# Performance work log

Measured on AMD Instinct MI355X. Metric: run time of the kernel, lower is better.

Reference implementation:

```python
import jax, jax.numpy as jnp
import numpy as np

N_BASIS = 16


def _kan_layer(x, coeffs, centers):
    # x: [b, in], coeffs: [out, in, n], centers: [n]
    mu = jnp.mean(x, axis=0)
    sd = jnp.std(x, axis=0, ddof=1)  # torch.std is unbiased by default
    xn = jnp.clip((x - mu) / (sd + 1e-6), -3.0, 3.0)
    # Gaussian RBF expansion: [b, in, n]
    basis = jnp.exp(-((xn[..., None] - centers) ** 2) / 0.5)
    return jnp.einsum('bin,oin->bo', basis, coeffs)


def setup_inputs() -> dict:
    key = jax.random.key(0)
    ks = jax.random.split(key, 6)
    B, IN, H = 16384, 256, 512
    return {
        'x': jax.random.normal(ks[0], (B, IN), jnp.float32),
        'coeffs1': jax.random.normal(ks[1], (H, IN, N_BASIS), jnp.float32) * 0.1,
        'coeffs2': jax.random.normal(ks[2], (H, H, N_BASIS), jnp.float32) * 0.1,
        'coeffs3': jax.random.normal(ks[3], (1, H, N_BASIS), jnp.float32) * 0.1,
        'skip_w': jax.random.normal(ks[4], (1, IN), jnp.float32) * 0.05,
        'skip_b': jnp.zeros((1,), jnp.float32),
    }


def reference(x, coeffs1, coeffs2, coeffs3, skip_w, skip_b):
    centers = jnp.linspace(-2.0, 2.0, N_BASIS).astype(x.dtype)
    h = jnp.tanh(_kan_layer(x, coeffs1, centers))
    h = jnp.tanh(_kan_layer(h, coeffs2, centers))
    out = _kan_layer(h, coeffs3, centers)[:, 0]  # squeeze(-1)
    skip = (x @ skip_w.T + skip_b)[:, 0]
    return out + skip
```

## Files before the change

kernel.cpp:

```cpp
#include <hip/hip_runtime.h>
#include <cstdint>
#include <cstddef>

typedef __attribute__((ext_vector_type(8))) _Float16 half8;
typedef __attribute__((ext_vector_type(4))) _Float16 half4;
typedef __attribute__((ext_vector_type(2))) __fp16   fp16x2;
typedef __attribute__((ext_vector_type(4))) float    floatx4;

static constexpr int B_ROWS = 16384;
static constexpr int IN_DIM = 256;
static constexpr int H_DIM  = 512;
static constexpr int NB     = 16;

__device__ __forceinline__ float fast_tanh(float x) {
  float ax = fabsf(x);
  float e  = __expf(2.0f * ax);
  float t  = 1.0f - 2.0f / (e + 1.0f);
  return copysignf(t, x);
}

__device__ __forceinline__ void gld16(const void* g, void* l) {
  __builtin_amdgcn_global_load_lds(
      (const __attribute__((address_space(1))) unsigned int*)g,
      (__attribute__((address_space(3))) unsigned int*)l, 16, 0, 0);
}

__global__ __launch_bounds__(256) void prep_k(const float* __restrict__ c1, _Float16* __restrict__ d1, size_t n41,
                                              const float* __restrict__ c2, _Float16* __restrict__ d2, size_t n42,
                                              const float* __restrict__ X,
                                              float* __restrict__ ps, float* __restrict__ ps2) {
  const int bx = blockIdx.x;
  if (bx < 128) {
    int c     = (bx & 3) * 64 + (threadIdx.x & 63);
    int chunk = threadIdx.x >> 6;
    int seg   = bx >> 2;
    int r0    = seg * 512;
    double s = 0.0, s2 = 0.0;
    for (int r = r0 + chunk; r < r0 + 512; r += 4) {
      float v = X[(size_t)r * IN_DIM + c];
      s += v; s2 += (double)v * (double)v;
    }
    __shared__ float Ls[256], Ls2[256];
    Ls[threadIdx.x] = (float)s; Ls2[threadIdx.x] = (float)s2;
    __syncthreads();
    if (chunk == 0) {
      int cl = threadIdx.x;
      float a  = Ls[cl]  + Ls[cl + 64]  + Ls[cl + 128]  + Ls[cl + 192];
      float b  = Ls2[cl] + Ls2[cl + 64] + Ls2[cl + 128] + Ls2[cl + 192];
      ps [(size_t)seg * IN_DIM + c] = a;
      ps2[(size_t)seg * IN_DIM + c] = b;
    }
  } else {
    size_t tot = n41 + n42;
    int nb_blocks = gridDim.x - 128;
    for (size_t i = (size_t)(bx - 128) * 256 + threadIdx.x; i < tot;
         i += (size_t)nb_blocks * 256) {
      const float4* sp; half4* dp; size_t j;
      if (i < n41) { sp = (const float4*)c1; dp = (half4*)d1; j = i; }
      else         { sp = (const float4*)c2; dp = (half4*)d2; j = i - n41; }
      float4 v = sp[j];
      int nb = (int)((j << 2) & 15);
      half4 r;
      float e0 = -2.f + (float)(nb + 0) * (4.f / 15.f);
      float e1 = -2.f + (float)(nb + 1) * (4.f / 15.f);
      float e2 = -2.f + (float)(nb + 2) * (4.f / 15.f);
      float e3 = -2.f + (float)(nb + 3) * (4.f / 15.f);
      r[0] = (_Float16)(v.x * __expf(-2.f * e0 * e0));
      r[1] = (_Float16)(v.y * __expf(-2.f * e1 * e1));
      r[2] = (_Float16)(v.z * __expf(-2.f * e2 * e2));
      r[3] = (_Float16)(v.w * __expf(-2.f * e3 * e3));
      dp[j] = r;
    }
  }
}

__global__ void stats_final_k(const float* __restrict__ ps,
                              const float* __restrict__ ps2,
                              int segs, int cols, int rows,
                              float* __restrict__ nmi, float* __restrict__ isd) {
  int c = blockIdx.x * blockDim.x + threadIdx.x;
  if (c >= cols) return;
  double s = 0.0, s2 = 0.0;
  for (int g = 0; g < segs; g++) { s += ps[(size_t)g * cols + c]; s2 += ps2[(size_t)g * cols + c]; }
  double mean = s / rows;
  double var  = (s2 - s * s / rows) / (rows - 1);
  if (var < 0.0) var = 0.0;
  float sd = (float)sqrt(var);
  float iv = 1.0f / (sd + 1e-6f);
  isd[c] = iv;
  nmi[c] = -(float)mean * iv;
}

__global__ __launch_bounds__(256, 2) void kan_gemm_fused(const float* __restrict__ X,
                                                         const float* __restrict__ nmi,
                                                         const float* __restrict__ isd,
                                                         const _Float16* __restrict__ Bm,
                                                         float* __restrict__ Hout,
                                                         float* __restrict__ psum,
                                                         float* __restrict__ psum2,
                                                         int C) {
  const int K = C << 4;
  const int steps = K >> 6;
  __shared__ __align__(16) _Float16 As[2][128 * 64];
  __shared__ __align__(16) _Float16 Bs[2][128 * 64];
  __shared__ float Rs1[2][128], Rs2[2][128];
  const int tid  = threadIdx.x;
  const int w = tid >> 6, lane = tid & 63;
  const int wm = w & 1, wn = w >> 1;
  const int lrow = lane & 15, quad = lane >> 4;
  const int row0 = blockIdx.x * 128;
  const int col0 = blockIdx.y * 128;

  const int s_row = tid >> 3;
  const int s_sl  = tid & 7;
  const int s_seg = s_sl ^ ((s_row >> 1) & 7);
  const _Float16* gB = Bm + (size_t)(col0 + s_row) * K + s_seg * 8;

  const int erow = tid >> 1, eh = tid & 1;
  const float* xp  = X   + (size_t)(row0 + erow) * C + 2 * eh;
  const float* mup = nmi + 2 * eh;
  const float* isp = isd + 2 * eh;

  floatx4 acc[4][4] = {};

  auto expand_store = [&](float2 v, float2 a, float2 b, int bufi) {
#pragma unroll
    for (int h = 0; h < 2; h++) {
      float xr = h ? v.y : v.x;
      float ii = h ? a.y : a.x;
      float bb = h ? b.y : b.x;
      float xn = fminf(fmaxf(fmaf(xr, ii, bb), -3.f), 3.f);
      float Wv = __expf(fmaf(-2.f, xn, -8.f) * xn);
      float g  = __expf((16.f / 15.f) * xn);
      float g2 = g * g, g4 = g2 * g2, g8 = g4 * g4;
      fp16x2 gg = __builtin_amdgcn_cvt_pkrtz(g2, g2);
      union { fp16x2 q[4]; half8 v8; } u0, u1;
      u0.q[0] = __builtin_amdgcn_cvt_pkrtz(Wv, Wv * g);
      u0.q[1] = u0.q[0] * gg;
      u0.q[2] = u0.q[1] * gg;
      u0.q[3] = u0.q[2] * gg;
      float W8 = Wv * g8;
      u1.q[0] = __builtin_amdgcn_cvt_pkrtz(W8, W8 * g);
      u1.q[1] = u1.q[0] * gg;
      u1.q[2] = u1.q[1] * gg;
      u1.q[3] = u1.q[2] * gg;
      int ks0 = 4 * eh + 2 * h;
      *(half8*)&As[bufi][(size_t)(ks0 * 128 + erow) * 8]       = u0.v8;
      *(half8*)&As[bufi][(size_t)((ks0 + 1) * 128 + erow) * 8] = u1.v8;
    }
  };

#pragma unroll
  for (int i = 0; i < 4; i++)
    gld16(gB + (size_t)32 * i * K, &Bs[0][(size_t)(tid + 256 * i) * 8]);
  expand_store(*(const float2*)xp, *(const float2*)isp, *(const float2*)mup, 0);
  float2 xv = {}, av = {}, bv = {};
  if (steps > 1) {
    xv = *(const float2*)(xp + 4);
    av = *(const float2*)(isp + 4);
    bv = *(const float2*)(mup + 4);
  }
  __syncthreads();

  for (int k = 0; k < steps; k++) {
    const int buf = k & 1, nb = buf ^ 1;
    const bool more = (k + 1 < steps);
    if (more) {
#pragma unroll
      for (int i = 0; i < 4; i++)
        gld16(gB + (size_t)(k + 1) * 64 + (size_t)32 * i * K,
              &Bs[nb][(size_t)(tid + 256 * i) * 8]);
    }
    half8 af0[4], bf0[4];
#pragma unroll
    for (int t = 0; t < 4; t++) {
      int arow = wm * 64 + t * 16 + lrow;
      af0[t] = *(const half8*)&As[buf][(size_t)(quad * 128 + arow) * 8];
      int brow = wn * 64 + t * 16 + lrow;
      int bchunk = brow * 8 + (quad ^ ((brow >> 1) & 7));
      bf0[t] = *(const half8*)&Bs[buf][(size_t)bchunk * 8];
    }
    __builtin_amdgcn_s_setprio(1);
#pragma unroll
    for (int tm = 0; tm < 4; tm++)
#pragma unroll
      for (int tn = 0; tn < 4; tn++)
        acc[tm][tn] = __builtin_amdgcn_mfma_f32_16x16x32_f16(af0[tm], bf0[tn], acc[tm][tn], 0, 0, 0);
    __builtin_amdgcn_s_setprio(0);
    if (more) {
      expand_store(xv, av, bv, nb);
      if (k + 2 < steps) {
        xv = *(const float2*)(xp + 4 * (k + 2));
        av = *(const float2*)(isp + 4 * (k + 2));
        bv = *(const float2*)(mup + 4 * (k + 2));
      }
    }
    half8 af1[4], bf1[4];
#pragma unroll
    for (int t = 0; t < 4; t++) {
      int arow = wm * 64 + t * 16 + lrow;
      af1[t] = *(const half8*)&As[buf][(size_t)((4 + quad) * 128 + arow) * 8];
      int brow = wn * 64 + t * 16 + lrow;
      int bchunk = brow * 8 + ((4 + quad) ^ ((brow >> 1) & 7));
      bf1[t] = *(const half8*)&Bs[buf][(size_t)bchunk * 8];
    }
    __builtin_amdgcn_s_setprio(1);
#pragma unroll
    for (int tm = 0; tm < 4; tm++)
#pragma unroll
      for (int tn = 0; tn < 4; tn++)
        acc[tm][tn] = __builtin_amdgcn_mfma_f32_16x16x32_f16(af1[tm], bf1[tn], acc[tm][tn], 0, 0, 0);
    __builtin_amdgcn_s_setprio(0);
    __syncthreads();
  }

  float s1[4] = {0.f, 0.f, 0.f, 0.f}, s2v[4] = {0.f, 0.f, 0.f, 0.f};
#pragma unroll
  for (int tm = 0; tm < 4; tm++) {
#pragma unroll
    for (int tn = 0; tn < 4; tn++) {
      int gcol = col0 + wn * 64 + tn * 16 + lrow;
#pragma unroll
      for (int r = 0; r < 4; r++) {
        int grow = row0 + wm * 64 + tm * 16 + quad * 4 + r;
        float v = fast_tanh(acc[tm][tn][r]);
        Hout[(size_t)grow * H_DIM + gcol] = v;
        s1[tn] += v; s2v[tn] += v * v;
      }
    }
  }
#pragma unroll
  for (int tn = 0; tn < 4; tn++) {
    s1[tn]  += __shfl_xor(s1[tn], 16);  s1[tn]  += __shfl_xor(s1[tn], 32);
    s2v[tn] += __shfl_xor(s2v[tn], 16); s2v[tn] += __shfl_xor(s2v[tn], 32);
  }
  if (quad == 0) {
#pragma unroll
    for (int tn = 0; tn < 4; tn++) {
      Rs1[wm][wn * 64 + tn * 16 + lrow] = s1[tn];
      Rs2[wm][wn * 64 + tn * 16 + lrow] = s2v[tn];
    }
  }
  __syncthreads();
  if (tid < 128) {
    psum [(size_t)blockIdx.x * H_DIM + col0 + tid] = Rs1[0][tid] + Rs1[1][tid];
    psum2[(size_t)blockIdx.x * H_DIM + col0 + tid] = Rs2[0][tid] + Rs2[1][tid];
  }
}

__global__ __launch_bounds__(256) void layer3_k(const float* __restrict__ H2,
                                                const float* __restrict__ nmi,
                                                const float* __restrict__ isd,
                                                const float* __restrict__ C3,
                                                const float* __restrict__ X,
                                                const float* __restrict__ SW,
                                                const float* __restrict__ SB,
                                                float* __restrict__ OUT) {
  int w = threadIdx.x >> 6, lane = threadIdx.x & 63;
  float Kn[NB];
#pragma unroll
  for (int n = 0; n < NB; n++) {
    float c = -2.f + (float)n * (4.f / 15.f);
    Kn[n] = __expf(-2.f * c * c);
  }
  float sb0 = SB[0];
  int row_base = blockIdx.x * 16 + w * 4;
  for (int r = 0; r < 4; r++) {
    int row = row_base + r;
    float s = 0.f;
#pragma unroll
    for (int j = 0; j < 8; j++) {
      int i = lane + 64 * j;
      float hv = H2[(size_t)row * H_DIM + i];
      float xn = fminf(fmaxf(fmaf(hv, isd[i], nmi[i]), -3.f), 3.f);
      float Wf = __expf(fmaf(-2.f, xn, -8.f) * xn);
      float gf = __expf((16.f / 15.f) * xn);
      const floatx4* cp = (const floatx4*)(C3 + (size_t)i * NB);
      floatx4 c0 = cp[0], c1 = cp[1], c2 = cp[2], c3 = cp[3];
      float p = Wf;
#pragma unroll
      for (int n = 0; n < 4; n++) { s += p * Kn[n]      * c0[n]; p *= gf; }
#pragma unroll
      for (int n = 0; n < 4; n++) { s += p * Kn[n + 4]  * c1[n]; p *= gf; }
#pragma unroll
      for (int n = 0; n < 4; n++) { s += p * Kn[n + 8]  * c2[n]; p *= gf; }
#pragma unroll
      for (int n = 0; n < 4; n++) { s += p * Kn[n + 12] * c3[n]; p *= gf; }
    }
#pragma unroll
    for (int j = 0; j < 4; j++) {
      int i = lane + 64 * j;
      s += X[(size_t)row * IN_DIM + i] * SW[i];
    }
#pragma unroll
    for (int off = 32; off > 0; off >>= 1) s += __shfl_down(s, off);
    if (lane == 0) OUT[row] = s + sb0;
  }
}

extern "C" void kernel_launch(void* const* d_in, const int* in_sizes, int n_in,
                              void* d_out, int out_size, void* d_ws, size_t ws_size,
                              hipStream_t stream) {
  const float* x  = (const float*)d_in[0];
  const float* c1 = (const float*)d_in[1];
  const float* c2 = (const float*)d_in[2];
  const float* c3 = (const float*)d_in[3];
  const float* sw = (const float*)d_in[4];
  const float* sb = (const float*)d_in[5];
  float* out = (float*)d_out;

  const int B = B_ROWS, IN = IN_DIM, H = H_DIM;

  char* ws = (char*)d_ws;
  size_t off = 0;
  auto alloc = [&](size_t bytes) -> void* {
    void* p = ws + off;
    off += (bytes + 255) & ~(size_t)255;
    return p;
  };
  _Float16* C1h = (_Float16*)alloc((size_t)H * IN * NB * 2);
  _Float16* C2h = (_Float16*)alloc((size_t)H * H  * NB * 2);
  float* H1 = (float*)alloc((size_t)B * H * 4);
  float* H2 = (float*)alloc((size_t)B * H * 4);
  float* ps  = (float*)alloc(128 * 512 * 4);
  float* ps2 = (float*)alloc(128 * 512 * 4);
  float* nmi = (float*)alloc(512 * 4);
  float* isd = (float*)alloc(512 * 4);

  prep_k<<<128 + 1024, 256, 0, stream>>>(c1, C1h, (size_t)H * IN * NB / 4,
                                         c2, C2h, (size_t)H * H * NB / 4,
                                         x, ps, ps2);
  stats_final_k<<<1, 256, 0, stream>>>(ps, ps2, 32, IN, B, nmi, isd);

  kan_gemm_fused<<<dim3(B / 128, 4), 256, 0, stream>>>(x, nmi, isd, C1h, H1, ps, ps2, IN);
  stats_final_k<<<2, 256, 0, stream>>>(ps, ps2, 128, H, B, nmi, isd);

  kan_gemm_fused<<<dim3(B / 128, 4), 256, 0, stream>>>(H1, nmi, isd, C2h, H2, ps, ps2, H);
  stats_final_k<<<2, 256, 0, stream>>>(ps, ps2, 128, H, B, nmi, isd);

  layer3_k<<<B / 16, 256, 0, stream>>>(H2, nmi, isd, c3, x, sw, sb, out);
}
```

Before: 455.6 us.

## Triple-buffer B tiles with prefetch distance two and manual waitcnt barriers

The weight (B) tile shared buffer grows from two to three stages, so global-to-LDS loads are issued two K-steps ahead instead of one. Each `__syncthreads` is replaced with an explicit `lgkmcnt` wait plus `s_barrier`, so the barrier no longer waits on outstanding vector-memory loads. The reduction scratch reuses the A buffer, so total LDS grows only by one B stage. The intent is to hide more global-memory latency behind the MFMA work. The cost is higher LDS use, which may limit occupancy, and ordering now relies on hand-placed waits and in-order `vmcnt` retirement rather than full syncs.

Result: no change. 454.6 us (-0.2%).

```diff
diff --git a/kernel.cpp b/kernel.cpp
--- a/kernel.cpp
+++ b/kernel.cpp
@@ -102,8 +102,7 @@
   const int K = C << 4;
   const int steps = K >> 6;
   __shared__ __align__(16) _Float16 As[2][128 * 64];
-  __shared__ __align__(16) _Float16 Bs[2][128 * 64];
-  __shared__ float Rs1[2][128], Rs2[2][128];
+  __shared__ __align__(16) _Float16 Bs[3][128 * 64];
   const int tid  = threadIdx.x;
   const int w = tid >> 6, lane = tid & 63;
   const int wm = w & 1, wn = w >> 1;
@@ -150,35 +149,47 @@
     }
   };
 
+  float2 x0 = *(const float2*)xp;
+  float2 a0 = *(const float2*)isp;
+  float2 b0 = *(const float2*)mup;
 #pragma unroll
   for (int i = 0; i < 4; i++)
     gld16(gB + (size_t)32 * i * K, &Bs[0][(size_t)(tid + 256 * i) * 8]);
-  expand_store(*(const float2*)xp, *(const float2*)isp, *(const float2*)mup, 0);
-  float2 xv = {}, av = {}, bv = {};
-  if (steps > 1) {
-    xv = *(const float2*)(xp + 4);
-    av = *(const float2*)(isp + 4);
-    bv = *(const float2*)(mup + 4);
-  }
-  __syncthreads();
-
+  __builtin_amdgcn_sched_barrier(0);
+#pragma unroll
+  for (int i = 0; i < 4; i++)
+    gld16(gB + 64 + (size_t)32 * i * K, &Bs[1][(size_t)(tid + 256 * i) * 8]);
+  __builtin_amdgcn_sched_barrier(0);
+  float2 xv = *(const float2*)(xp + 4);
+  float2 av = *(const float2*)(isp + 4);
+  float2 bv = *(const float2*)(mup + 4);
+  expand_store(x0, a0, b0, 0);
+  asm volatile("s_waitcnt vmcnt(7)" ::: "memory");
+  asm volatile("s_waitcnt lgkmcnt(0)" ::: "memory");
+  __builtin_amdgcn_s_barrier();
+  __builtin_amdgcn_sched_barrier(0);
+
+  int bcur = 0;
   for (int k = 0; k < steps; k++) {
-    const int buf = k & 1, nb = buf ^ 1;
-    const bool more = (k + 1 < steps);
-    if (more) {
+    const int abuf = k & 1;
+    const bool more  = (k + 1 < steps);
+    const bool more2 = (k + 2 < steps);
+    const int b2 = (bcur == 0) ? 2 : bcur - 1;
+    if (more2) {
 #pragma unroll
       for (int i = 0; i < 4; i++)
-        gld16(gB + (size_t)(k + 1) * 64 + (size_t)32 * i * K,
-              &Bs[nb][(size_t)(tid + 256 * i) * 8]);
+        gld16(gB + (size_t)(k + 2) * 64 + (size_t)32 * i * K,
+              &Bs[b2][(size_t)(tid + 256 * i) * 8]);
+      __builtin_amdgcn_sched_barrier(0);
     }
     half8 af0[4], bf0[4];
 #pragma unroll
     for (int t = 0; t < 4; t++) {
       int arow = wm * 64 + t * 16 + lrow;
-      af0[t] = *(const half8*)&As[buf][(size_t)(quad * 128 + arow) * 8];
+      af0[t] = *(const half8*)&As[abuf][(size_t)(quad * 128 + arow) * 8];
       int brow = wn * 64 + t * 16 + lrow;
       int bchunk = brow * 8 + (quad ^ ((brow >> 1) & 7));
-      bf0[t] = *(const half8*)&Bs[buf][(size_t)bchunk * 8];
+      bf0[t] = *(const half8*)&Bs[bcur][(size_t)bchunk * 8];
     }
     __builtin_amdgcn_s_setprio(1);
 #pragma unroll
@@ -188,8 +199,8 @@
         acc[tm][tn] = __builtin_amdgcn_mfma_f32_16x16x32_f16(af0[tm], bf0[tn], acc[tm][tn], 0, 0, 0);
     __builtin_amdgcn_s_setprio(0);
     if (more) {
-      expand_store(xv, av, bv, nb);
-      if (k + 2 < steps) {
+      expand_store(xv, av, bv, abuf ^ 1);
+      if (more2) {
         xv = *(const float2*)(xp + 4 * (k + 2));
         av = *(const float2*)(isp + 4 * (k + 2));
         bv = *(const float2*)(mup + 4 * (k + 2));
@@ -199,10 +210,10 @@
 #pragma unroll
     for (int t = 0; t < 4; t++) {
       int arow = wm * 64 + t * 16 + lrow;
-      af1[t] = *(const half8*)&As[buf][(size_t)((4 + quad) * 128 + arow) * 8];
+      af1[t] = *(const half8*)&As[abuf][(size_t)((4 + quad) * 128 + arow) * 8];
       int brow = wn * 64 + t * 16 + lrow;
       int bchunk = brow * 8 + ((4 + quad) ^ ((brow >> 1) & 7));
-      bf1[t] = *(const half8*)&Bs[buf][(size_t)bchunk * 8];
+      bf1[t] = *(const half8*)&Bs[bcur][(size_t)bchunk * 8];
     }
     __builtin_amdgcn_s_setprio(1);
 #pragma unroll
@@ -211,9 +222,14 @@
       for (int tn = 0; tn < 4; tn++)
         acc[tm][tn] = __builtin_amdgcn_mfma_f32_16x16x32_f16(af1[tm], bf1[tn], acc[tm][tn], 0, 0, 0);
     __builtin_amdgcn_s_setprio(0);
-    __syncthreads();
-  }
-
+    asm volatile("s_waitcnt lgkmcnt(0)" ::: "memory");
+    __builtin_amdgcn_s_barrier();
+    __builtin_amdgcn_sched_barrier(0);
+    bcur = (bcur == 2) ? 0 : bcur + 1;
+  }
+
+  float* Rs1 = reinterpret_cast<float*>(&As[0][0]);
+  float* Rs2 = Rs1 + 256;
   float s1[4] = {0.f, 0.f, 0.f, 0.f}, s2v[4] = {0.f, 0.f, 0.f, 0.f};
 #pragma unroll
   for (int tm = 0; tm < 4; tm++) {
@@ -237,14 +253,16 @@
   if (quad == 0) {
 #pragma unroll
     for (int tn = 0; tn < 4; tn++) {
-      Rs1[wm][wn * 64 + tn * 16 + lrow] = s1[tn];
-      Rs2[wm][wn * 64 + tn * 16 + lrow] = s2v[tn];
-    }
-  }
-  __syncthreads();
+      Rs1[wm * 128 + wn * 64 + tn * 16 + lrow] = s1[tn];
+      Rs2[wm * 128 + wn * 64 + tn * 16 + lrow] = s2v[tn];
+    }
+  }
+  asm volatile("s_waitcnt lgkmcnt(0)" ::: "memory");
+  __builtin_amdgcn_s_barrier();
+  __builtin_amdgcn_sched_barrier(0);
   if (tid < 128) {
-    psum [(size_t)blockIdx.x * H_DIM + col0 + tid] = Rs1[0][tid] + Rs1[1][tid];
-    psum2[(size_t)blockIdx.x * H_DIM + col0 + tid] = Rs2[0][tid] + Rs2[1][tid];
+    psum [(size_t)blockIdx.x * H_DIM + col0 + tid] = Rs1[tid] + Rs1[128 + tid];
+    psum2[(size_t)blockIdx.x * H_DIM + col0 + tid] = Rs2[tid] + Rs2[128 + tid];
   }
 }
 
```
